# Kernel tuning notes

Hardware: AMD Instinct MI355X
Metric: run time of the kernel (lower is better)

## Reference

```python
import jax, jax.numpy as jnp
import numpy as np

EPS = 1e-6
NUM_CHANNELS = 8


def rotate_half(x):
    h = x.shape[-1] // 2
    return jnp.concatenate([-x[..., h:], x[..., :h]], axis=-1)


def l1_normalize(x):
    # torch F.normalize(p=1): x / max(||x||_1, eps) along last dim
    n = jnp.sum(jnp.abs(x), axis=-1, keepdims=True)
    return x / jnp.maximum(n, EPS)


def squared_softmax(x):      # potential_func_z = 'square'
    return l1_normalize(x * x)


def abs_normalization(x):    # potential_func_g = 'abs'
    return l1_normalize(jax.nn.relu(x))


def head_selection(qz, u, v, cos, sin):
    b, s, d = qz.shape
    C = NUM_CHANNELS
    r = u.shape[0] // C
    cos_e = cos[:, None]  # [b,1,s,r] (unsqueeze_dim=1)
    sin_e = sin[:, None]
    ap = lambda x: x * cos_e + rotate_half(x) * sin_e
    ap_o = lambda x: x * cos_e - rotate_half(x) * sin_e
    # [b,s,C*r] -> [b,C,s,r]
    qz_u = (qz @ u.T).reshape(b, s, C, r).transpose(0, 2, 1, 3)
    qz_v = (qz @ v.T).reshape(b, s, C, r).transpose(0, 2, 1, 3)
    qz_uo = ap_o(qz_u)
    qz_u = ap(qz_u)
    qz_v = ap(qz_v)
    msg_F = jnp.einsum('bcqr,bckr->bcqk', qz_u, qz_v)          # [b,C,s,s]
    # regularize_h = 1/dim_z -> softmax(F * dim_z)
    qh = jax.nn.softmax(msg_F.astype(jnp.float32) * d, axis=-1).astype(qz_u.dtype)
    qh_v1 = jnp.einsum('bcqk,bckr->bcqr', qh, qz_v)
    qh_v2 = jnp.einsum('bcqk,bcqr->bckr', qh, qz_uo)           # qh^T @ qz_uo
    qh_v1 = ap_o(qh_v1).transpose(0, 2, 1, 3).reshape(b, s, C * r)
    qh_v2 = ap(qh_v2).transpose(0, 2, 1, 3).reshape(b, s, C * r)
    return qh_v1 @ u + qh_v2 @ v                               # ternary_factor_scaling = 1


def topic_modeling(qz, w):
    qg = abs_normalization(qz @ w.T)     # binary_factor_scaling = regularize_g = 1
    return qg @ w


def period_message(qz, period_mat, period_attn):
    # info = P @ qz @ A, single term since _lambda = 0
    return jnp.einsum('qk,bkd->bqd', period_mat, qz) @ period_attn


def reference(unary, cos, sin, ternary_u, ternary_v, binary_factor,
              period_mat, period_attn, num_iters):
    # mean-field iterator: qz = act_z((unary + messages)/regularize_z), regularize_z = 1
    qz = squared_softmax(unary)
    for _ in range(num_iters):
        msg = (head_selection(qz, ternary_u, ternary_v, cos, sin)
               + topic_modeling(qz, binary_factor)
               + period_message(qz, period_mat, period_attn))
        qz = squared_softmax(unary + msg)
    return qz


def setup_inputs() -> dict:
    key = jax.random.key(0)
    ks = jax.random.split(key, 4)
    b, s, d, dff = 2, 2048, 256, 1024
    C = NUM_CHANNELS
    r = d // C  # head_dim = 32
    unary = jax.random.normal(ks[0], (b, s, d), dtype=jnp.float32)
    # RoPE tables (theta = 10000)
    inv_freq = 1.0 / (10000.0 ** (np.arange(0, r, 2, dtype=np.float32) / r))
    pos = np.arange(s, dtype=np.float32)
    freqs = pos[:, None] * inv_freq[None, :]
    emb = np.concatenate([freqs, freqs], axis=-1)               # [s, r]
    cos = jnp.broadcast_to(jnp.asarray(np.cos(emb))[None], (b, s, r)).astype(jnp.float32)
    sin = jnp.broadcast_to(jnp.asarray(np.sin(emb))[None], (b, s, r)).astype(jnp.float32)
    std = 0.2
    ternary_u = jax.random.normal(ks[1], (C * r, d), dtype=jnp.float32) * std
    ternary_v = jax.random.normal(ks[2], (C * r, d), dtype=jnp.float32) * std
    binary_factor = jax.random.normal(ks[3], (dff, d), dtype=jnp.float32) * std
    # PTPeriod buffers: band |i-j| == 24, and decaying matrix (k=1 -> identity)
    i = np.arange(s)
    period_mat = jnp.asarray((np.abs(i[:, None] - i[None, :]) == 24).astype(np.float32))
    j = np.arange(d)
    dist = np.abs(j[:, None] - j[None, :]).astype(np.float32)
    attn = np.exp(-0.5 * dist ** 2)
    attn[dist >= 1.0] = 0.0
    period_attn = jnp.asarray(attn, dtype=jnp.float32)
    return {"unary": unary, "cos": cos, "sin": sin,
            "ternary_u": ternary_u, "ternary_v": ternary_v,
            "binary_factor": binary_factor,
            "period_mat": period_mat, "period_attn": period_attn,
            "num_iters": 3}
```

## Files before the change

### kernel.cpp

```cpp
#include <hip/hip_runtime.h>
#include <math.h>

#define B 2
#define S 2048
#define D 256
#define DFF 1024
#define NC 8
#define R 32
#define NITER 3
#define EPSV 1e-6f
#define MROW (B * S)
#define NSPLIT 4

typedef unsigned short u16;
typedef unsigned int u32;
typedef __attribute__((ext_vector_type(8))) short short8_t;
typedef __attribute__((ext_vector_type(4))) float f32x4;

#define MFMA16(a, b, c) __builtin_amdgcn_mfma_f32_16x16x32_bf16(a, b, c, 0, 0, 0)

__device__ inline u16 bf16_rne(float x) {
  u32 u = __float_as_uint(x);
  u32 r = u + 0x7FFFu + ((u >> 16) & 1u);
  return (u16)(r >> 16);
}
__device__ inline void split2(float x, u16& h, u16& l) {
  h = bf16_rne(x);
  float hf = __uint_as_float(((u32)h) << 16);
  l = bf16_rne(x - hf);
}
__device__ inline short8_t ld8(const u16* p) { return *(const short8_t*)p; }

__device__ inline u32 pk2(float a, float b) {
  u32 r;
  asm("v_cvt_pk_bf16_f32 %0, %1, %2" : "=v"(r) : "v"(a), "v"(b));
  return r;
}
__device__ inline short8_t pack8(float c0, float c1, float c2, float c3,
                                 float c4, float c5, float c6, float c7) {
  union { u32 w[4]; short8_t v; } u_;
  u_.w[0] = pk2(c0, c1);
  u_.w[1] = pk2(c2, c3);
  u_.w[2] = pk2(c4, c5);
  u_.w[3] = pk2(c6, c7);
  return u_.v;
}

__device__ inline void gload_lds16(const u16* g, u16* l) {
  __builtin_amdgcn_global_load_lds(
      (const __attribute__((address_space(1))) unsigned int*)g,
      (__attribute__((address_space(3))) unsigned int*)l, 16, 0, 0);
}

__global__ __launch_bounds__(256) void k_sqsm(const float* __restrict__ unary,
                                              const float* __restrict__ msgs,
                                              const float* __restrict__ qzp,
                                              const int* __restrict__ pcols,
                                              const float* __restrict__ pvals,
                                              const int* __restrict__ pcnt,
                                              float* __restrict__ outf,
                                              u16* __restrict__ qzz) {
  int row = blockIdx.x;
  int t = threadIdx.x;
  int i = row * D + t;
  float x = unary[i];
  if (msgs) {
    const size_t NEl = (size_t)MROW * D;
#pragma unroll
    for (int p = 0; p < NSPLIT; p++) x += msgs[p * NEl + i];
    int b = row >> 11, q = row & 2047;
    int n = pcnt[q];
    for (int j = 0; j < n; j++)
      x = fmaf(pvals[q * 16 + j], qzp[(size_t)(b * S + pcols[q * 16 + j]) * D + t], x);
  }
  float v = x * x;
  float s = v;
#pragma unroll
  for (int off = 32; off; off >>= 1) s += __shfl_down(s, off, 64);
  __shared__ float red[4];
  if ((t & 63) == 0) red[t >> 6] = s;
  __syncthreads();
  float tot = fmaxf(red[0] + red[1] + red[2] + red[3], EPSV);
  float y = v / tot;
  if (outf) outf[i] = y;
  u16 h, l;
  split2(y, h, l);
  size_t rb = (size_t)row * 512;
  qzz[rb + t] = h;
  qzz[rb + 256 + t] = l;
}

__global__ __launch_bounds__(256) void k_gemm_z(
    const u16* __restrict__ Az, const u16* __restrict__ Bz,
    int K2, int Kpart, int N,
    float* __restrict__ outbase,
    float* __restrict__ quv, float* __restrict__ qg, float* __restrict__ qzp) {
  int Kh = K2 / 3;
  int Alda = Kh * 2;
  int m0 = blockIdx.x * 128, n0 = blockIdx.y * 128;
  int kbeg = blockIdx.z * Kpart, kend = kbeg + Kpart;
  int tid = threadIdx.x;
  int wid = tid >> 6, lane = tid & 63;
  int lr = lane & 15, lg = lane >> 4;
  int wm = (wid >> 1) * 64, wn = (wid & 1) * 64;

  __shared__ alignas(16) u16 As[8192];
  __shared__ alignas(16) u16 Bs[8192];

  f32x4 acc[4][4];
#pragma unroll
  for (int fr = 0; fr < 4; fr++)
#pragma unroll
    for (int fc = 0; fc < 4; fc++) acc[fr][fc] = (f32x4){0.f, 0.f, 0.f, 0.f};

  for (int kk = kbeg; kk < kend; kk += 64) {
    int zsrc = (kk >= Kh) ? kk - Kh : kk;
    __syncthreads();
#pragma unroll
    for (int it = 0; it < 4; it++) {
      int f = (it * 256 + tid) * 16;
      int row = f >> 7;
      int c16 = ((f >> 4) & 7) ^ (row & 7);
      u16* ldst = (u16*)As + it * 2048 + wid * 512;
      gload_lds16(Az + (size_t)(m0 + row) * Alda + zsrc + c16 * 8, ldst);
      u16* ldstB = (u16*)Bs + it * 2048 + wid * 512;
      gload_lds16(Bz + (size_t)(n0 + row) * K2 + kk + c16 * 8, ldstB);
    }
    __syncthreads();
#pragma unroll
    for (int ks = 0; ks < 2; ks++) {
      int cb = ks * 4 + lg;
      int sw = (cb ^ (lr & 7)) << 3;
      short8_t af[4], bf[4];
#pragma unroll
      for (int fr = 0; fr < 4; fr++)
        af[fr] = *(const short8_t*)(As + ((wm + fr * 16 + lr) << 6) + sw);
#pragma unroll
      for (int fc = 0; fc < 4; fc++)
        bf[fc] = *(const short8_t*)(Bs + ((wn + fc * 16 + lr) << 6) + sw);
      __builtin_amdgcn_s_setprio(1);
#pragma unroll
      for (int fr = 0; fr < 4; fr++)
#pragma unroll
        for (int fc = 0; fc < 4; fc++)
          acc[fr][fc] = MFMA16(af[fr], bf[fc], acc[fr][fc]);
      __builtin_amdgcn_s_setprio(0);
    }
  }

  if (qg) {
#pragma unroll
    for (int fr = 0; fr < 4; fr++)
#pragma unroll
      for (int fc = 0; fc < 4; fc++)
#pragma unroll
        for (int i = 0; i < 4; i++) {
          int m = m0 + wm + fr * 16 + lg * 4 + i;
          int nn = n0 + wn + fc * 16 + lr;
          float x = acc[fr][fc][i];
          if (nn < 512) quv[(size_t)m * 512 + nn] = x;
          else if (nn < 1536) qg[(size_t)m * DFF + nn - 512] = fmaxf(x, 0.f);
          else qzp[(size_t)m * 256 + nn - 1536] = x;
        }
  } else {
    float* out = outbase + (size_t)blockIdx.z * ((size_t)gridDim.x * 128) * N;
#pragma unroll
    for (int fr = 0; fr < 4; fr++)
#pragma unroll
      for (int fc = 0; fc < 4; fc++)
#pragma unroll
        for (int i = 0; i < 4; i++) {
          int m = m0 + wm + fr * 16 + lg * 4 + i;
          int nn = n0 + wn + fc * 16 + lr;
          out[(size_t)m * N + nn] = acc[fr][fc][i];
        }
  }
}

__global__ __launch_bounds__(256) void k_rope_pre(
    const float* __restrict__ quv, const float* __restrict__ cosb,
    const float* __restrict__ sinb,
    u16* __restrict__ Ah, u16* __restrict__ Al,
    u16* __restrict__ Bvh, u16* __restrict__ Bvl,
    u16* __restrict__ BvTph, u16* __restrict__ AoTph) {
  int row = blockIdx.x;
  int b = row >> 11, s_ = row & 2047;
  int t = threadIdx.x, c = t >> 5, rr = t & 31;
  float qu = quv[(size_t)row * 512 + t];
  float qv = quv[(size_t)row * 512 + 256 + t];
  float ou = __shfl_xor(qu, 16, 64);
  float ov = __shfl_xor(qv, 16, 64);
  float ru = (rr < 16) ? -ou : ou;
  float rv = (rr < 16) ? -ov : ov;
  float cs = cosb[(size_t)(b * S + s_) * R + rr];
  float sn = sinb[(size_t)(b * S + s_) * R + rr];
  float a = (qu * cs + ru * sn) * 256.f;
  float ao = qu * cs - ru * sn;
  float bv = qv * cs + rv * sn;
  size_t o = ((size_t)(b * NC + c) * S + s_) * R + rr;
  int off = s_ & 63;
  int kt = off >> 4;
  int pp = (kt >> 1) * 32 + ((off >> 2) & 3) * 8 + (kt & 1) * 4 + (off & 3);
  size_t otp = ((size_t)(b * NC + c) * R + rr) * S + (size_t)((s_ & ~63) + pp);
  u16 h, l;
  split2(a, h, l);  Ah[o] = h;  Al[o] = l;
  split2(bv, h, l); Bvh[o] = h; Bvl[o] = l; BvTph[otp] = h;
  split2(ao, h, l); AoTph[otp] = h;
}

__global__ __launch_bounds__(512) void k_attn1_mfma(
    const u16* __restrict__ Ah, const u16* __restrict__ Al,
    const u16* __restrict__ Bvh, const u16* __restrict__ Bvl,
    const u16* __restrict__ BvTph,
    float* __restrict__ O1, float* __restrict__ mbuf, float* __restrict__ lbuf) {
  int bidx = blockIdx.x;
  int xcd = bidx & 7, wv = bidx >> 3;
  int bc = xcd * 2 + (wv & 1);
  int tile = wv >> 1;
  int tid = threadIdx.x;
  int wid = tid >> 6, lane = tid & 63;
  int lr = lane & 15, lg = lane >> 4;
  int w4 = wid & 3, kh = wid >> 2;
  int qr = tile * 128 + w4 * 32;
  const size_t ofs = (size_t)bc * S * R;
  const size_t ofsT = (size_t)bc * R * S;

  __shared__ alignas(16) u16 BvhS[2][2][2048];
  __shared__ alignas(16) u16 BvlS[2][2][2048];
  __shared__ alignas(16) u16 PvS[2][2][2048];
  __shared__ float cm_o[4][32][34];
  __shared__ float cm_m[4][32], cm_l[4][32];

  short8_t a_hi[2], a_lo[2];
#pragma unroll
  for (int t = 0; t < 2; t++) {
    a_hi[t] = ld8(Ah + ofs + (size_t)(qr + t * 16 + lr) * R + lg * 8);
    a_lo[t] = ld8(Al + ofs + (size_t)(qr + t * 16 + lr) * R + lg * 8);
  }

  f32x4 o[2][2];
#pragma unroll
  for (int t = 0; t < 2; t++) { o[t][0] = (f32x4){0,0,0,0}; o[t][1] = (f32x4){0,0,0,0}; }
  float m_q[2] = {-1e30f, -1e30f}, l_p[2] = {0.f, 0.f};

  int khs = tid >> 8;
  int pch = tid & 255;
  int r4 = pch >> 2, c4 = pch & 3;
  int r8 = pch >> 3, c8 = pch & 7;
  int wql = (wid & 3) * 512;

#define A1_STAGE(STEP, DB)                                                     \
  {                                                                            \
    int kb_ = khs * 1024 + (STEP) * 64;                                        \
    gload_lds16(Bvh + ofs + (size_t)(kb_ + r4) * R + c4 * 8, &BvhS[DB][khs][wql]); \
    gload_lds16(Bvl + ofs + (size_t)(kb_ + r4) * R + c4 * 8, &BvlS[DB][khs][wql]); \
    gload_lds16(BvTph + ofsT + (size_t)r8 * S + kb_ + c8 * 8, &PvS[DB][khs][wql]); \
  }

  A1_STAGE(0, 0);
  for (int step = 0; step < 16; step++) {
    int db = step & 1;
    __syncthreads();
    if (step + 1 < 16) A1_STAGE(step + 1, db ^ 1);

    short8_t sbH[4], sbL[4], pvb[4];
#pragma unroll
    for (int kt = 0; kt < 4; kt++) {
      int ro = (kt * 16 + lr) * 32 + lg * 8;
      sbH[kt] = ld8(&BvhS[db][kh][ro]);
      sbL[kt] = ld8(&BvlS[db][kh][ro]);
    }
#pragma unroll
    for (int j = 0; j < 4; j++)
      pvb[j] = ld8(&PvS[db][kh][((j & 1) * 16 + lr) * 64 + (j >> 1) * 32 + lg * 8]);

    f32x4 c[2][4];
    __builtin_amdgcn_s_setprio(1);
#pragma unroll
    for (int t = 0; t < 2; t++)
#pragma unroll
      for (int kt = 0; kt < 4; kt++) {
        f32x4 cc = {0.f, 0.f, 0.f, 0.f};
        cc = MFMA16(sbH[kt], a_hi[t], cc);
        cc = MFMA16(sbH[kt], a_lo[t], cc);
        cc = MFMA16(sbL[kt], a_hi[t], cc);
        c[t][kt] = cc;
      }
    __builtin_amdgcn_s_setprio(0);
    float mx0 = -1e30f, mx1 = -1e30f;
#pragma unroll
    for (int kt = 0; kt < 4; kt++)
#pragma unroll
      for (int i = 0; i < 4; i++) {
        mx0 = fmaxf(mx0, c[0][kt][i]);
        mx1 = fmaxf(mx1, c[1][kt][i]);
      }
    bool ok_ = (mx0 <= m_q[0] + 8.f) && (mx1 <= m_q[1] + 8.f);
    if (!__all((int)ok_)) {
#pragma unroll
      for (int t = 0; t < 2; t++) {
        float mxt = (t == 0) ? mx0 : mx1;
        mxt = fmaxf(mxt, __shfl_xor(mxt, 16, 64));
        mxt = fmaxf(mxt, __shfl_xor(mxt, 32, 64));
        float mnew = fmaxf(m_q[t], mxt);
        float sc = __expf(m_q[t] - mnew);
        m_q[t] = mnew;
        l_p[t] *= sc;
#pragma unroll
        for (int i = 0; i < 4; i++) {
          float s4 = __shfl(sc, (lane & 48) | (lg * 4 + i), 64);
          o[t][0][i] *= s4;
          o[t][1][i] *= s4;
        }
      }
    }
#pragma unroll
    for (int t = 0; t < 2; t++) {
      float ps = 0.f;
#pragma unroll
      for (int kt = 0; kt < 4; kt++)
#pragma unroll
        for (int i = 0; i < 4; i++) {
          c[t][kt][i] = __expf(c[t][kt][i] - m_q[t]);
          ps += c[t][kt][i];
        }
      l_p[t] += ps;
    }
    __builtin_amdgcn_s_setprio(1);
#pragma unroll
    for (int t = 0; t < 2; t++) {
      short8_t f0h = pack8(c[t][0][0], c[t][0][1], c[t][0][2], c[t][0][3],
                           c[t][1][0], c[t][1][1], c[t][1][2], c[t][1][3]);
      short8_t f1h = pack8(c[t][2][0], c[t][2][1], c[t][2][2], c[t][2][3],
                           c[t][3][0], c[t][3][1], c[t][3][2], c[t][3][3]);
      o[t][0] = MFMA16(f0h, pvb[0], o[t][0]);
      o[t][1] = MFMA16(f0h, pvb[1], o[t][1]);
      o[t][0] = MFMA16(f1h, pvb[2], o[t][0]);
      o[t][1] = MFMA16(f1h, pvb[3], o[t][1]);
    }
    __builtin_amdgcn_s_setprio(0);
  }

  float m4[2][4], l4[2][4];
#pragma unroll
  for (int t = 0; t < 2; t++) {
    float lq = l_p[t];
    lq += __shfl_xor(lq, 16, 64);
    lq += __shfl_xor(lq, 32, 64);
#pragma unroll
    for (int i = 0; i < 4; i++) {
      int src = (lane & 48) | (lg * 4 + i);
      m4[t][i] = __shfl(m_q[t], src, 64);
      l4[t][i] = __shfl(lq, src, 64);
    }
  }
  __syncthreads();
  if (kh == 1) {
#pragma unroll
    for (int t = 0; t < 2; t++)
#pragma unroll
      for (int i = 0; i < 4; i++) {
        int r_ = t * 16 + lg * 4 + i;
        cm_o[w4][r_][lr] = o[t][0][i];
        cm_o[w4][r_][lr + 16] = o[t][1][i];
        if (lr == 0) { cm_m[w4][r_] = m4[t][i]; cm_l[w4][r_] = l4[t][i]; }
      }
  }
  __syncthreads();
  if (kh == 0) {
#pragma unroll
    for (int t = 0; t < 2; t++)
#pragma unroll
      for (int i = 0; i < 4; i++) {
        int r_ = t * 16 + lg * 4 + i;
        int q = qr + r_;
        float mb = cm_m[w4][r_], lb = cm_l[w4][r_];
        float mN = fmaxf(m4[t][i], mb);
        float ea = __expf(m4[t][i] - mN), eb = __expf(mb - mN);
        float inv = 1.f / (l4[t][i] * ea + lb * eb);
        O1[ofs + (size_t)q * R + lr] = (o[t][0][i] * ea + cm_o[w4][r_][lr] * eb) * inv;
        O1[ofs + (size_t)q * R + 16 + lr] = (o[t][1][i] * ea + cm_o[w4][r_][lr + 16] * eb) * inv;
        if (lr == 0) {
          mbuf[(size_t)bc * S + q] = mN;
          lbuf[(size_t)bc * S + q] = inv;
        }
      }
  }
}

__global__ __launch_bounds__(512) void k_attn2_mfma(
    const u16* __restrict__ Ah, const u16* __restrict__ Al,
    const u16* __restrict__ Bvh, const u16* __restrict__ Bvl,
    const u16* __restrict__ AoTph,
    const float* __restrict__ mbuf, const float* __restrict__ lbuf,
    float* __restrict__ O2) {
  int bidx = blockIdx.x;
  int xcd = bidx & 7, wv = bidx >> 3;
  int bc = xcd * 2 + (wv & 1);
  int tile = wv >> 1;
  int tid = threadIdx.x;
  int wid = tid >> 6, lane = tid & 63;
  int lr = lane & 15, lg = lane >> 4;
  int w4 = wid & 3, qh = wid >> 2;
  int kr = tile * 128 + w4 * 32;
  const size_t ofs = (size_t)bc * S * R;
  const size_t ofsT = (size_t)bc * R * S;

  __shared__ alignas(16) u16 AhS[2][2][2048];
  __shared__ alignas(16) u16 AlS[2][2][2048];
  __shared__ alignas(16) u16 PvS[2][2][2048];
  __shared__ float cm[4][32][34];

  short8_t bv_hi[2], bv_lo[2];
#pragma unroll
  for (int t = 0; t < 2; t++) {
    bv_hi[t] = ld8(Bvh + ofs + (size_t)(kr + t * 16 + lr) * R + lg * 8);
    bv_lo[t] = ld8(Bvl + ofs + (size_t)(kr + t * 16 + lr) * R + lg * 8);
  }

  f32x4 o[2][2];
#pragma unroll
  for (int t = 0; t < 2; t++) { o[t][0] = (f32x4){0,0,0,0}; o[t][1] = (f32x4){0,0,0,0}; }

  int qhs = tid >> 8;
  int pch = tid & 255;
  int r4 = pch >> 2, c4 = pch & 3;
  int r8 = pch >> 3, c8 = pch & 7;
  int wql = (wid & 3) * 512;

#define A2_STAGE(STEP, DB)                                                     \
  {                                                                            \
    int qb_ = qhs * 1024 + (STEP) * 64;                                        \
    gload_lds16(Ah + ofs + (size_t)(qb_ + r4) * R + c4 * 8, &AhS[DB][qhs][wql]);   \
    gload_lds16(Al + ofs + (size_t)(qb_ + r4) * R + c4 * 8, &AlS[DB][qhs][wql]);   \
    gload_lds16(AoTph + ofsT + (size_t)r8 * S + qb_ + c8 * 8, &PvS[DB][qhs][wql]); \
  }

  A2_STAGE(0, 0);
  for (int step = 0; step < 16; step++) {
    int db = step & 1;
    __syncthreads();
    if (step + 1 < 16) A2_STAGE(step + 1, db ^ 1);

    short8_t saH[4], saL[4], pvb[4];
#pragma unroll
    for (int qt = 0; qt < 4; qt++) {
      int ro = (qt * 16 + lr) * 32 + lg * 8;
      saH[qt] = ld8(&AhS[db][qh][ro]);
      saL[qt] = ld8(&AlS[db][qh][ro]);
    }
#pragma unroll
    for (int j = 0; j < 4; j++)
      pvb[j] = ld8(&PvS[db][qh][((j & 1) * 16 + lr) * 64 + (j >> 1) * 32 + lg * 8]);

    f32x4 c[2][4];
    __builtin_amdgcn_s_setprio(1);
#pragma unroll
    for (int t = 0; t < 2; t++)
#pragma unroll
      for (int qt = 0; qt < 4; qt++) {
        f32x4 cc = {0.f, 0.f, 0.f, 0.f};
        cc = MFMA16(saH[qt], bv_hi[t], cc);
        cc = MFMA16(saH[qt], bv_lo[t], cc);
        cc = MFMA16(saL[qt], bv_hi[t], cc);
        c[t][qt] = cc;
      }
    __builtin_amdgcn_s_setprio(0);
    size_t qa = (size_t)bc * S + qh * 1024 + step * 64;
    float4 mq0 = *(const float4*)(mbuf + qa + lg * 4);
    float4 mq1 = *(const float4*)(mbuf + qa + 16 + lg * 4);
    float4 mq2 = *(const float4*)(mbuf + qa + 32 + lg * 4);
    float4 mq3 = *(const float4*)(mbuf + qa + 48 + lg * 4);
    float4 il0 = *(const float4*)(lbuf + qa + lg * 4);
    float4 il1 = *(const float4*)(lbuf + qa + 16 + lg * 4);
    float4 il2 = *(const float4*)(lbuf + qa + 32 + lg * 4);
    float4 il3 = *(const float4*)(lbuf + qa + 48 + lg * 4);
#pragma unroll
    for (int t = 0; t < 2; t++) {
      c[t][0][0] = __expf(c[t][0][0] - mq0.x) * il0.x;
      c[t][0][1] = __expf(c[t][0][1] - mq0.y) * il0.y;
      c[t][0][2] = __expf(c[t][0][2] - mq0.z) * il0.z;
      c[t][0][3] = __expf(c[t][0][3] - mq0.w) * il0.w;
      c[t][1][0] = __expf(c[t][1][0] - mq1.x) * il1.x;
      c[t][1][1] = __expf(c[t][1][1] - mq1.y) * il1.y;
      c[t][1][2] = __expf(c[t][1][2] - mq1.z) * il1.z;
      c[t][1][3] = __expf(c[t][1][3] - mq1.w) * il1.w;
      c[t][2][0] = __expf(c[t][2][0] - mq2.x) * il2.x;
      c[t][2][1] = __expf(c[t][2][1] - mq2.y) * il2.y;
      c[t][2][2] = __expf(c[t][2][2] - mq2.z) * il2.z;
      c[t][2][3] = __expf(c[t][2][3] - mq2.w) * il2.w;
      c[t][3][0] = __expf(c[t][3][0] - mq3.x) * il3.x;
      c[t][3][1] = __expf(c[t][3][1] - mq3.y) * il3.y;
      c[t][3][2] = __expf(c[t][3][2] - mq3.z) * il3.z;
      c[t][3][3] = __expf(c[t][3][3] - mq3.w) * il3.w;
    }
    __builtin_amdgcn_s_setprio(1);
#pragma unroll
    for (int t = 0; t < 2; t++) {
      short8_t f0h = pack8(c[t][0][0], c[t][0][1], c[t][0][2], c[t][0][3],
                           c[t][1][0], c[t][1][1], c[t][1][2], c[t][1][3]);
      short8_t f1h = pack8(c[t][2][0], c[t][2][1], c[t][2][2], c[t][2][3],
                           c[t][3][0], c[t][3][1], c[t][3][2], c[t][3][3]);
      o[t][0] = MFMA16(f0h, pvb[0], o[t][0]);
      o[t][1] = MFMA16(f0h, pvb[1], o[t][1]);
      o[t][0] = MFMA16(f1h, pvb[2], o[t][0]);
      o[t][1] = MFMA16(f1h, pvb[3], o[t][1]);
    }
    __builtin_amdgcn_s_setprio(0);
  }

  __syncthreads();
  if (qh == 1) {
#pragma unroll
    for (int t = 0; t < 2; t++)
#pragma unroll
      for (int i = 0; i < 4; i++) {
        int r_ = t * 16 + lg * 4 + i;
        cm[w4][r_][lr] = o[t][0][i];
        cm[w4][r_][lr + 16] = o[t][1][i];
      }
  }
  __syncthreads();
  if (qh == 0) {
#pragma unroll
    for (int t = 0; t < 2; t++)
#pragma unroll
      for (int i = 0; i < 4; i++) {
        int r_ = t * 16 + lg * 4 + i;
        int k = kr + r_;
        O2[ofs + (size_t)k * R + lr] = o[t][0][i] + cm[w4][r_][lr];
        O2[ofs + (size_t)k * R + 16 + lr] = o[t][1][i] + cm[w4][r_][lr + 16];
      }
  }
}

__global__ __launch_bounds__(256) void k_post(const float* __restrict__ O1,
                                              const float* __restrict__ O2,
                                              const float* __restrict__ cosb,
                                              const float* __restrict__ sinb,
                                              const float* __restrict__ qg,
                                              u16* __restrict__ Abz) {
  int row = blockIdx.x;
  int b = row >> 11, s_ = row & 2047;
  int t = threadIdx.x, c = t >> 5, rr = t & 31;
  size_t base = ((size_t)(b * NC + c) * S + s_) * R;
  float x1 = O1[base + rr], x2 = O2[base + rr];
  float o1 = O1[base + (rr ^ 16)], o2 = O2[base + (rr ^ 16)];
  float r1 = (rr < 16) ? -o1 : o1;
  float r2 = (rr < 16) ? -o2 : o2;
  float cs = cosb[(size_t)(b * S + s_) * R + rr];
  float sn = sinb[(size_t)(b * S + s_) * R + rr];
  float v1 = x1 * cs - r1 * sn;
  float v2 = x2 * cs + r2 * sn;
  size_t rb = (size_t)row * 3072;
  u16 h, l;
  split2(v1, h, l);
  Abz[rb + t] = h;        Abz[rb + 1536 + t] = l;
  split2(v2, h, l);
  Abz[rb + 256 + t] = h;  Abz[rb + 1792 + t] = l;
  float vq[4];
  float s = 0.f;
#pragma unroll
  for (int j = 0; j < 4; j++) {
    vq[j] = qg[(size_t)row * DFF + t + 256 * j];
    s += vq[j];
  }
#pragma unroll
  for (int off = 32; off; off >>= 1) s += __shfl_down(s, off, 64);
  __shared__ float red[4];
  if ((t & 63) == 0) red[t >> 6] = s;
  __syncthreads();
  float inv = 1.f / fmaxf(red[0] + red[1] + red[2] + red[3], EPSV);
#pragma unroll
  for (int j = 0; j < 4; j++) {
    split2(vq[j] * inv, h, l);
    Abz[rb + 512 + t + 256 * j] = h;
    Abz[rb + 2048 + t + 256 * j] = l;
  }
}

__global__ __launch_bounds__(256) void k_prep_bt(const float* __restrict__ u,
                                                 const float* __restrict__ v,
                                                 const float* __restrict__ w,
                                                 const float* __restrict__ pa,
                                                 u16* __restrict__ btz) {
  int n = blockIdx.x;
  int k = threadIdx.x;
  float val = (n < 256)    ? u[(size_t)n * 256 + k]
            : (n < 512)    ? v[(size_t)(n - 256) * 256 + k]
            : (n < 1536)   ? w[(size_t)(n - 512) * 256 + k]
                           : pa[(size_t)k * 256 + (n - 1536)];
  u16 h, l;
  split2(val, h, l);
  size_t rb = (size_t)n * 768;
  btz[rb + k] = h;
  btz[rb + 256 + k] = l;
  btz[rb + 512 + k] = h;
}

__global__ __launch_bounds__(256) void k_prep_uvwT(const float* __restrict__ u,
                                                   const float* __restrict__ v,
                                                   const float* __restrict__ w,
                                                   u16* __restrict__ uvwTz) {
  int n = blockIdx.x;
  size_t rb = (size_t)n * 4608;
  for (int k = threadIdx.x; k < 1536; k += 256) {
    float val = (k < 256) ? u[(size_t)k * 256 + n]
              : (k < 512) ? v[(size_t)(k - 256) * 256 + n]
                          : w[(size_t)(k - 512) * 256 + n];
    u16 h, l;
    split2(val, h, l);
    uvwTz[rb + k] = h;
    uvwTz[rb + 1536 + k] = l;
    uvwTz[rb + 3072 + k] = h;
  }
}

__global__ __launch_bounds__(256) void k_pm_build(const float* __restrict__ pm,
                                                  int* __restrict__ cols,
                                                  float* __restrict__ vals,
                                                  int* __restrict__ cnt) {
  int q = blockIdx.x;
  int t = threadIdx.x;
  float v[8];
  int c = 0;
#pragma unroll
  for (int j = 0; j < 8; j++) {
    v[j] = pm[(size_t)q * S + t * 8 + j];
    c += (v[j] != 0.f) ? 1 : 0;
  }
  int lane = t & 63, w = t >> 6;
  int pc = c;
#pragma unroll
  for (int off = 1; off < 64; off <<= 1) {
    int o = __shfl_up(pc, off, 64);
    if (lane >= off) pc += o;
  }
  __shared__ int wsum[4];
  if (lane == 63) wsum[w] = pc;
  __syncthreads();
  int base = 0;
  for (int i = 0; i < w; i++) base += wsum[i];
  int idx = base + pc - c;
#pragma unroll
  for (int j = 0; j < 8; j++) {
    if (v[j] != 0.f) {
      if (idx < 16) {
        cols[q * 16 + idx] = t * 8 + j;
        vals[q * 16 + idx] = v[j];
      }
      idx++;
    }
  }
  if (t == 255) {
    int tot = base + pc;
    cnt[q] = tot > 16 ? 16 : tot;
  }
}

extern "C" void kernel_launch(void* const* d_in, const int* in_sizes, int n_in,
                              void* d_out, int out_size, void* d_ws, size_t ws_size,
                              hipStream_t stream) {
  const float* unary = (const float*)d_in[0];
  const float* cosb = (const float*)d_in[1];
  const float* sinb = (const float*)d_in[2];
  const float* u = (const float*)d_in[3];
  const float* v = (const float*)d_in[4];
  const float* w = (const float*)d_in[5];
  const float* pm = (const float*)d_in[6];
  const float* pa = (const float*)d_in[7];

  const size_t NE = (size_t)MROW * D;
  const size_t NB = (size_t)B * NC * S * R;

  float* fp = (float*)d_ws;
  float* msgs = fp;                fp += NSPLIT * NE;
  float* quv = fp;                 fp += 2 * NE;
  float* qg = fp;                  fp += 4 * NE;
  float* qzp = fp;                 fp += NE;
  float* mbuf = fp;                fp += B * NC * S;
  float* lbuf = fp;                fp += B * NC * S;
  float* pvals = fp;               fp += S * 16;
  int* pcols = (int*)fp;           fp += S * 16;
  int* pcnt = (int*)fp;            fp += S;
  float* O1 = quv;
  float* O2 = quv + NE;

  u16* bb = (u16*)fp;
  u16* qzz = bb;                   bb += (size_t)MROW * 512;
  u16* Abz = bb;                   bb += (size_t)MROW * 3072;
  u16* btz = bb;                   bb += (size_t)1792 * 768;
  u16* uvwTz = bb;                 bb += (size_t)256 * 4608;
  u16* Ah = bb;                    bb += NB;
  u16* Al = bb;                    bb += NB;
  u16* Bvh = bb;                   bb += NB;
  u16* Bvl = bb;                   bb += NB;
  u16* BvTph = bb;                 bb += NB;
  u16* AoTph = bb;                 bb += NB;

  k_pm_build<<<S, 256, 0, stream>>>(pm, pcols, pvals, pcnt);
  k_prep_bt<<<1792, 256, 0, stream>>>(u, v, w, pa, btz);
  k_prep_uvwT<<<256, 256, 0, stream>>>(u, v, w, uvwTz);

  k_sqsm<<<MROW, 256, 0, stream>>>(unary, nullptr, nullptr, nullptr, nullptr, nullptr,
                                   nullptr, qzz);

  for (int it = 0; it < NITER; ++it) {
    k_gemm_z<<<dim3(32, 14, 1), 256, 0, stream>>>(qzz, btz, 768, 768, 1792,
                                                  nullptr, quv, qg, qzp);
    k_rope_pre<<<MROW, 256, 0, stream>>>(quv, cosb, sinb, Ah, Al, Bvh, Bvl, BvTph, AoTph);
    k_attn1_mfma<<<256, 512, 0, stream>>>(Ah, Al, Bvh, Bvl, BvTph, O1, mbuf, lbuf);
    k_attn2_mfma<<<256, 512, 0, stream>>>(Ah, Al, Bvh, Bvl, AoTph, mbuf, lbuf, O2);
    k_post<<<MROW, 256, 0, stream>>>(O1, O2, cosb, sinb, qg, Abz);
    k_gemm_z<<<dim3(32, 2, NSPLIT), 256, 0, stream>>>(Abz, uvwTz, 4608, 4608 / NSPLIT, 256,
                                                      msgs, nullptr, nullptr, nullptr);
    k_sqsm<<<MROW, 256, 0, stream>>>(unary, msgs, qzp, pcols, pvals, pcnt,
                                     (it == NITER - 1) ? (float*)d_out : nullptr, qzz);
  }
}
```

Measured before the change: 454.2 us.

## Double waves per attention block, one 16-row tile per wave

Both attention kernels now launch 1024 threads (16 waves) per block instead of 512. Each wave handles a 16-row query or key tile instead of two 16-row tiles, and the cooperative LDS staging loads are repartitioned across the larger wave count. The goal is more waves per CU to hide latency on the serial softmax/exp and MFMA chains. In exchange, the same shared tiles are re-read from LDS by twice as many waves, and per-wave MFMA work per LDS read is halved.

```diff
diff --git a/kernel.cpp b/kernel.cpp
--- a/kernel.cpp
+++ b/kernel.cpp
@@ -208,7 +208,7 @@
   split2(ao, h, l); AoTph[otp] = h;
 }
 
-__global__ __launch_bounds__(512) void k_attn1_mfma(
+__global__ __launch_bounds__(1024) void k_attn1_mfma(
     const u16* __restrict__ Ah, const u16* __restrict__ Al,
     const u16* __restrict__ Bvh, const u16* __restrict__ Bvl,
     const u16* __restrict__ BvTph,
@@ -218,43 +218,41 @@
   int bc = xcd * 2 + (wv & 1);
   int tile = wv >> 1;
   int tid = threadIdx.x;
-  int wid = tid >> 6, lane = tid & 63;
+  int lane = tid & 63;
   int lr = lane & 15, lg = lane >> 4;
-  int w4 = wid & 3, kh = wid >> 2;
-  int qr = tile * 128 + w4 * 32;
+  int khs = tid >> 9;
+  int w8 = (tid >> 6) & 7;
+  int qr = tile * 128 + w8 * 16;
   const size_t ofs = (size_t)bc * S * R;
   const size_t ofsT = (size_t)bc * R * S;
 
   __shared__ alignas(16) u16 BvhS[2][2][2048];
   __shared__ alignas(16) u16 BvlS[2][2][2048];
   __shared__ alignas(16) u16 PvS[2][2][2048];
-  __shared__ float cm_o[4][32][34];
-  __shared__ float cm_m[4][32], cm_l[4][32];
-
-  short8_t a_hi[2], a_lo[2];
-#pragma unroll
-  for (int t = 0; t < 2; t++) {
-    a_hi[t] = ld8(Ah + ofs + (size_t)(qr + t * 16 + lr) * R + lg * 8);
-    a_lo[t] = ld8(Al + ofs + (size_t)(qr + t * 16 + lr) * R + lg * 8);
-  }
-
-  f32x4 o[2][2];
-#pragma unroll
-  for (int t = 0; t < 2; t++) { o[t][0] = (f32x4){0,0,0,0}; o[t][1] = (f32x4){0,0,0,0}; }
-  float m_q[2] = {-1e30f, -1e30f}, l_p[2] = {0.f, 0.f};
-
-  int khs = tid >> 8;
-  int pch = tid & 255;
-  int r4 = pch >> 2, c4 = pch & 3;
-  int r8 = pch >> 3, c8 = pch & 7;
-  int wql = (wid & 3) * 512;
-
-#define A1_STAGE(STEP, DB)                                                     \
-  {                                                                            \
-    int kb_ = khs * 1024 + (STEP) * 64;                                        \
-    gload_lds16(Bvh + ofs + (size_t)(kb_ + r4) * R + c4 * 8, &BvhS[DB][khs][wql]); \
-    gload_lds16(Bvl + ofs + (size_t)(kb_ + r4) * R + c4 * 8, &BvlS[DB][khs][wql]); \
-    gload_lds16(BvTph + ofsT + (size_t)r8 * S + kb_ + c8 * 8, &PvS[DB][khs][wql]); \
+  __shared__ float cm_o[8][16][34];
+  __shared__ float cm_m[8][16], cm_l[8][16];
+
+  short8_t a_hi = ld8(Ah + ofs + (size_t)(qr + lr) * R + lg * 8);
+  short8_t a_lo = ld8(Al + ofs + (size_t)(qr + lr) * R + lg * 8);
+
+  f32x4 o0 = {0, 0, 0, 0}, o1 = {0, 0, 0, 0};
+  float m_q = -1e30f, l_p = 0.f;
+
+  int ci = (w8 & 3) * 64 + lane;
+  int wql = (w8 & 3) * 512;
+
+#define A1_STAGE(STEP, DB)                                                         \
+  {                                                                                \
+    int kb_ = khs * 1024 + (STEP) * 64;                                            \
+    if (w8 < 4) {                                                                  \
+      gload_lds16(Bvh + ofs + (size_t)(kb_ + (ci >> 2)) * R + (ci & 3) * 8,        \
+                  &BvhS[DB][khs][wql]);                                            \
+      gload_lds16(BvTph + ofsT + (size_t)(ci >> 3) * S + kb_ + (ci & 7) * 8,       \
+                  &PvS[DB][khs][wql]);                                             \
+    } else {                                                                       \
+      gload_lds16(Bvl + ofs + (size_t)(kb_ + (ci >> 2)) * R + (ci & 3) * 8,        \
+                  &BvlS[DB][khs][wql]);                                            \
+    }                                                                              \
   }
 
   A1_STAGE(0, 0);
@@ -267,128 +265,105 @@
 #pragma unroll
     for (int kt = 0; kt < 4; kt++) {
       int ro = (kt * 16 + lr) * 32 + lg * 8;
-      sbH[kt] = ld8(&BvhS[db][kh][ro]);
-      sbL[kt] = ld8(&BvlS[db][kh][ro]);
+      sbH[kt] = ld8(&BvhS[db][khs][ro]);
+      sbL[kt] = ld8(&BvlS[db][khs][ro]);
     }
 #pragma unroll
     for (int j = 0; j < 4; j++)
-      pvb[j] = ld8(&PvS[db][kh][((j & 1) * 16 + lr) * 64 + (j >> 1) * 32 + lg * 8]);
-
-    f32x4 c[2][4];
+      pvb[j] = ld8(&PvS[db][khs][((j & 1) * 16 + lr) * 64 + (j >> 1) * 32 + lg * 8]);
+
+    f32x4 c[4];
     __builtin_amdgcn_s_setprio(1);
 #pragma unroll
-    for (int t = 0; t < 2; t++)
-#pragma unroll
-      for (int kt = 0; kt < 4; kt++) {
-        f32x4 cc = {0.f, 0.f, 0.f, 0.f};
-        cc = MFMA16(sbH[kt], a_hi[t], cc);
-        cc = MFMA16(sbH[kt], a_lo[t], cc);
-        cc = MFMA16(sbL[kt], a_hi[t], cc);
-        c[t][kt] = cc;
+    for (int kt = 0; kt < 4; kt++) {
+      f32x4 cc = {0.f, 0.f, 0.f, 0.f};
+      cc = MFMA16(sbH[kt], a_hi, cc);
+      cc = MFMA16(sbH[kt], a_lo, cc);
+      cc = MFMA16(sbL[kt], a_hi, cc);
+      c[kt] = cc;
+    }
+    __builtin_amdgcn_s_setprio(0);
+    float mx = -1e30f;
+#pragma unroll
+    for (int kt = 0; kt < 4; kt++)
+#pragma unroll
+      for (int i = 0; i < 4; i++) mx = fmaxf(mx, c[kt][i]);
+    if (!__all((int)(mx <= m_q + 8.f))) {
+      mx = fmaxf(mx, __shfl_xor(mx, 16, 64));
+      mx = fmaxf(mx, __shfl_xor(mx, 32, 64));
+      float mnew = fmaxf(m_q, mx);
+      float sc = __expf(m_q - mnew);
+      m_q = mnew;
+      l_p *= sc;
+#pragma unroll
+      for (int i = 0; i < 4; i++) {
+        float s4 = __shfl(sc, (lane & 48) | (lg * 4 + i), 64);
+        o0[i] *= s4;
+        o1[i] *= s4;
       }
+    }
+    float ps = 0.f;
+#pragma unroll
+    for (int kt = 0; kt < 4; kt++)
+#pragma unroll
+      for (int i = 0; i < 4; i++) {
+        c[kt][i] = __expf(c[kt][i] - m_q);
+        ps += c[kt][i];
+      }
+    l_p += ps;
+    __builtin_amdgcn_s_setprio(1);
+    short8_t f0h = pack8(c[0][0], c[0][1], c[0][2], c[0][3],
+                         c[1][0], c[1][1], c[1][2], c[1][3]);
+    short8_t f1h = pack8(c[2][0], c[2][1], c[2][2], c[2][3],
+                         c[3][0], c[3][1], c[3][2], c[3][3]);
+    o0 = MFMA16(f0h, pvb[0], o0);
+    o1 = MFMA16(f0h, pvb[1], o1);
+    o0 = MFMA16(f1h, pvb[2], o0);
+    o1 = MFMA16(f1h, pvb[3], o1);
     __builtin_amdgcn_s_setprio(0);
-    float mx0 = -1e30f, mx1 = -1e30f;
-#pragma unroll
-    for (int kt = 0; kt < 4; kt++)
-#pragma unroll
-      for (int i = 0; i < 4; i++) {
-        mx0 = fmaxf(mx0, c[0][kt][i]);
-        mx1 = fmaxf(mx1, c[1][kt][i]);
+  }
+
+  float lq = l_p;
+  lq += __shfl_xor(lq, 16, 64);
+  lq += __shfl_xor(lq, 32, 64);
+  float m4[4], l4[4];
+#pragma unroll
+  for (int i = 0; i < 4; i++) {
+    int src = (lane & 48) | (lg * 4 + i);
+    m4[i] = __shfl(m_q, src, 64);
+    l4[i] = __shfl(lq, src, 64);
+  }
+  __syncthreads();
+  if (khs == 1) {
+#pragma unroll
+    for (int i = 0; i < 4; i++) {
+      int r_ = lg * 4 + i;
+      cm_o[w8][r_][lr] = o0[i];
+      cm_o[w8][r_][lr + 16] = o1[i];
+      if (lr == 0) { cm_m[w8][r_] = m4[i]; cm_l[w8][r_] = l4[i]; }
+    }
+  }
+  __syncthreads();
+  if (khs == 0) {
+#pragma unroll
+    for (int i = 0; i < 4; i++) {
+      int r_ = lg * 4 + i;
+      int q = qr + r_;
+      float mb = cm_m[w8][r_], lb = cm_l[w8][r_];
+      float mN = fmaxf(m4[i], mb);
+      float ea = __expf(m4[i] - mN), eb = __expf(mb - mN);
+      float inv = 1.f / (l4[i] * ea + lb * eb);
+      O1[ofs + (size_t)q * R + lr] = (o0[i] * ea + cm_o[w8][r_][lr] * eb) * inv;
+      O1[ofs + (size_t)q * R + 16 + lr] = (o1[i] * ea + cm_o[w8][r_][lr + 16] * eb) * inv;
+      if (lr == 0) {
+        mbuf[(size_t)bc * S + q] = mN;
+        lbuf[(size_t)bc * S + q] = inv;
       }
-    bool ok_ = (mx0 <= m_q[0] + 8.f) && (mx1 <= m_q[1] + 8.f);
-    if (!__all((int)ok_)) {
-#pragma unroll
-      for (int t = 0; t < 2; t++) {
-        float mxt = (t == 0) ? mx0 : mx1;
-        mxt = fmaxf(mxt, __shfl_xor(mxt, 16, 64));
-        mxt = fmaxf(mxt, __shfl_xor(mxt, 32, 64));
-        float mnew = fmaxf(m_q[t], mxt);
-        float sc = __expf(m_q[t] - mnew);
-        m_q[t] = mnew;
-        l_p[t] *= sc;
-#pragma unroll
-        for (int i = 0; i < 4; i++) {
-          float s4 = __shfl(sc, (lane & 48) | (lg * 4 + i), 64);
-          o[t][0][i] *= s4;
-          o[t][1][i] *= s4;
-        }
-      }
-    }
-#pragma unroll
-    for (int t = 0; t < 2; t++) {
-      float ps = 0.f;
-#pragma unroll
-      for (int kt = 0; kt < 4; kt++)
-#pragma unroll
-        for (int i = 0; i < 4; i++) {
-          c[t][kt][i] = __expf(c[t][kt][i] - m_q[t]);
-          ps += c[t][kt][i];
-        }
-      l_p[t] += ps;
-    }
-    __builtin_amdgcn_s_setprio(1);
-#pragma unroll
-    for (int t = 0; t < 2; t++) {
-      short8_t f0h = pack8(c[t][0][0], c[t][0][1], c[t][0][2], c[t][0][3],
-                           c[t][1][0], c[t][1][1], c[t][1][2], c[t][1][3]);
-      short8_t f1h = pack8(c[t][2][0], c[t][2][1], c[t][2][2], c[t][2][3],
-                           c[t][3][0], c[t][3][1], c[t][3][2], c[t][3][3]);
-      o[t][0] = MFMA16(f0h, pvb[0], o[t][0]);
-      o[t][1] = MFMA16(f0h, pvb[1], o[t][1]);
-      o[t][0] = MFMA16(f1h, pvb[2], o[t][0]);
-      o[t][1] = MFMA16(f1h, pvb[3], o[t][1]);
-    }
-    __builtin_amdgcn_s_setprio(0);
-  }
-
-  float m4[2][4], l4[2][4];
-#pragma unroll
-  for (int t = 0; t < 2; t++) {
-    float lq = l_p[t];
-    lq += __shfl_xor(lq, 16, 64);
-    lq += __shfl_xor(lq, 32, 64);
-#pragma unroll
-    for (int i = 0; i < 4; i++) {
-      int src = (lane & 48) | (lg * 4 + i);
-      m4[t][i] = __shfl(m_q[t], src, 64);
-      l4[t][i] = __shfl(lq, src, 64);
-    }
-  }
-  __syncthreads();
-  if (kh == 1) {
-#pragma unroll
-    for (int t = 0; t < 2; t++)
-#pragma unroll
-      for (int i = 0; i < 4; i++) {
-        int r_ = t * 16 + lg * 4 + i;
-        cm_o[w4][r_][lr] = o[t][0][i];
-        cm_o[w4][r_][lr + 16] = o[t][1][i];
-        if (lr == 0) { cm_m[w4][r_] = m4[t][i]; cm_l[w4][r_] = l4[t][i]; }
-      }
-  }
-  __syncthreads();
-  if (kh == 0) {
-#pragma unroll
-    for (int t = 0; t < 2; t++)
-#pragma unroll
-      for (int i = 0; i < 4; i++) {
-        int r_ = t * 16 + lg * 4 + i;
-        int q = qr + r_;
-        float mb = cm_m[w4][r_], lb = cm_l[w4][r_];
-        float mN = fmaxf(m4[t][i], mb);
-        float ea = __expf(m4[t][i] - mN), eb = __expf(mb - mN);
-        float inv = 1.f / (l4[t][i] * ea + lb * eb);
-        O1[ofs + (size_t)q * R + lr] = (o[t][0][i] * ea + cm_o[w4][r_][lr] * eb) * inv;
-        O1[ofs + (size_t)q * R + 16 + lr] = (o[t][1][i] * ea + cm_o[w4][r_][lr + 16] * eb) * inv;
-        if (lr == 0) {
-          mbuf[(size_t)bc * S + q] = mN;
-          lbuf[(size_t)bc * S + q] = inv;
-        }
-      }
-  }
-}
-
-__global__ __launch_bounds__(512) void k_attn2_mfma(
+    }
+  }
+}
+
+__global__ __launch_bounds__(1024) void k_attn2_mfma(
     const u16* __restrict__ Ah, const u16* __restrict__ Al,
     const u16* __restrict__ Bvh, const u16* __restrict__ Bvl,
     const u16* __restrict__ AoTph,
@@ -399,41 +374,39 @@
   int bc = xcd * 2 + (wv & 1);
   int tile = wv >> 1;
   int tid = threadIdx.x;
-  int wid = tid >> 6, lane = tid & 63;
+  int lane = tid & 63;
   int lr = lane & 15, lg = lane >> 4;
-  int w4 = wid & 3, qh = wid >> 2;
-  int kr = tile * 128 + w4 * 32;
+  int qhs = tid >> 9;
+  int w8 = (tid >> 6) & 7;
+  int kr = tile * 128 + w8 * 16;
   const size_t ofs = (size_t)bc * S * R;
   const size_t ofsT = (size_t)bc * R * S;
 
   __shared__ alignas(16) u16 AhS[2][2][2048];
   __shared__ alignas(16) u16 AlS[2][2][2048];
   __shared__ alignas(16) u16 PvS[2][2][2048];
-  __shared__ float cm[4][32][34];
-
-  short8_t bv_hi[2], bv_lo[2];
-#pragma unroll
-  for (int t = 0; t < 2; t++) {
-    bv_hi[t] = ld8(Bvh + ofs + (size_t)(kr + t * 16 + lr) * R + lg * 8);
-    bv_lo[t] = ld8(Bvl + ofs + (size_t)(kr + t * 16 + lr) * R + lg * 8);
-  }
-
-  f32x4 o[2][2];
-#pragma unroll
-  for (int t = 0; t < 2; t++) { o[t][0] = (f32x4){0,0,0,0}; o[t][1] = (f32x4){0,0,0,0}; }
-
-  int qhs = tid >> 8;
-  int pch = tid & 255;
-  int r4 = pch >> 2, c4 = pch & 3;
-  int r8 = pch >> 3, c8 = pch & 7;
-  int wql = (wid & 3) * 512;
-
-#define A2_STAGE(STEP, DB)                                                     \
-  {                                                                            \
-    int qb_ = qhs * 1024 + (STEP) * 64;                                        \
-    gload_lds16(Ah + ofs + (size_t)(qb_ + r4) * R + c4 * 8, &AhS[DB][qhs][wql]);   \
-    gload_lds16(Al + ofs + (size_t)(qb_ + r4) * R + c4 * 8, &AlS[DB][qhs][wql]);   \
-    gload_lds16(AoTph + ofsT + (size_t)r8 * S + qb_ + c8 * 8, &PvS[DB][qhs][wql]); \
+  __shared__ float cm[8][16][34];
+
+  short8_t bv_hi = ld8(Bvh + ofs + (size_t)(kr + lr) * R + lg * 8);
+  short8_t bv_lo = ld8(Bvl + ofs + (size_t)(kr + lr) * R + lg * 8);
+
+  f32x4 o0 = {0, 0, 0, 0}, o1 = {0, 0, 0, 0};
+
+  int ci = (w8 & 3) * 64 + lane;
+  int wql = (w8 & 3) * 512;
+
+#define A2_STAGE(STEP, DB)                                                         \
+  {                                                                                \
+    int qb_ = qhs * 1024 + (STEP) * 64;                                            \
+    if (w8 < 4) {                                                                  \
+      gload_lds16(Ah + ofs + (size_t)(qb_ + (ci >> 2)) * R + (ci & 3) * 8,         \
+                  &AhS[DB][qhs][wql]);                                             \
+      gload_lds16(AoTph + ofsT + (size_t)(ci >> 3) * S + qb_ + (ci & 7) * 8,       \
+                  &PvS[DB][qhs][wql]);                                             \
+    } else {                                                                       \
+      gload_lds16(Al + ofs + (size_t)(qb_ + (ci >> 2)) * R + (ci & 3) * 8,         \
+                  &AlS[DB][qhs][wql]);                                             \
+    }                                                                              \
   }
 
   A2_STAGE(0, 0);
@@ -446,27 +419,25 @@
 #pragma unroll
     for (int qt = 0; qt < 4; qt++) {
       int ro = (qt * 16 + lr) * 32 + lg * 8;
-      saH[qt] = ld8(&AhS[db][qh][ro]);
-      saL[qt] = ld8(&AlS[db][qh][ro]);
+      saH[qt] = ld8(&AhS[db][qhs][ro]);
+      saL[qt] = ld8(&AlS[db][qhs][ro]);
     }
 #pragma unroll
     for (int j = 0; j < 4; j++)
-      pvb[j] = ld8(&PvS[db][qh][((j & 1) * 16 + lr) * 64 + (j >> 1) * 32 + lg * 8]);
-
-    f32x4 c[2][4];
+      pvb[j] = ld8(&PvS[db][qhs][((j & 1) * 16 + lr) * 64 + (j >> 1) * 32 + lg * 8]);
+
+    f32x4 c[4];
     __builtin_amdgcn_s_setprio(1);
 #pragma unroll
-    for (int t = 0; t < 2; t++)
-#pragma unroll
-      for (int qt = 0; qt < 4; qt++) {
-        f32x4 cc = {0.f, 0.f, 0.f, 0.f};
-        cc = MFMA16(saH[qt], bv_hi[t], cc);
-        cc = MFMA16(saH[qt], bv_lo[t], cc);
-        cc = MFMA16(saL[qt], bv_hi[t], cc);
-        c[t][qt] = cc;
-      }
+    for (int qt = 0; qt < 4; qt++) {
+      f32x4 cc = {0.f, 0.f, 0.f, 0.f};
+      cc = MFMA16(saH[qt], bv_hi, cc);
+      cc = MFMA16(saH[qt], bv_lo, cc);
+      cc = MFMA16(saL[qt], bv_hi, cc);
+      c[qt] = cc;
+    }
     __builtin_amdgcn_s_setprio(0);
-    size_t qa = (size_t)bc * S + qh * 1024 + step * 64;
+    size_t qa = (size_t)bc * S + qhs * 1024 + step * 64;
     float4 mq0 = *(const float4*)(mbuf + qa + lg * 4);
     float4 mq1 = *(const float4*)(mbuf + qa + 16 + lg * 4);
     float4 mq2 = *(const float4*)(mbuf + qa + 32 + lg * 4);
@@ -475,62 +446,52 @@
     float4 il1 = *(const float4*)(lbuf + qa + 16 + lg * 4);
     float4 il2 = *(const float4*)(lbuf + qa + 32 + lg * 4);
     float4 il3 = *(const float4*)(lbuf + qa + 48 + lg * 4);
-#pragma unroll
-    for (int t = 0; t < 2; t++) {
-      c[t][0][0] = __expf(c[t][0][0] - mq0.x) * il0.x;
-      c[t][0][1] = __expf(c[t][0][1] - mq0.y) * il0.y;
-      c[t][0][2] = __expf(c[t][0][2] - mq0.z) * il0.z;
-      c[t][0][3] = __expf(c[t][0][3] - mq0.w) * il0.w;
-      c[t][1][0] = __expf(c[t][1][0] - mq1.x) * il1.x;
-      c[t][1][1] = __expf(c[t][1][1] - mq1.y) * il1.y;
-      c[t][1][2] = __expf(c[t][1][2] - mq1.z) * il1.z;
-      c[t][1][3] = __expf(c[t][1][3] - mq1.w) * il1.w;
-      c[t][2][0] = __expf(c[t][2][0] - mq2.x) * il2.x;
-      c[t][2][1] = __expf(c[t][2][1] - mq2.y) * il2.y;
-      c[t][2][2] = __expf(c[t][2][2] - mq2.z) * il2.z;
-      c[t][2][3] = __expf(c[t][2][3] - mq2.w) * il2.w;
-      c[t][3][0] = __expf(c[t][3][0] - mq3.x) * il3.x;
-      c[t][3][1] = __expf(c[t][3][1] - mq3.y) * il3.y;
-      c[t][3][2] = __expf(c[t][3][2] - mq3.z) * il3.z;
-      c[t][3][3] = __expf(c[t][3][3] - mq3.w) * il3.w;
-    }
+    c[0][0] = __expf(c[0][0] - mq0.x) * il0.x;
+    c[0][1] = __expf(c[0][1] - mq0.y) * il0.y;
+    c[0][2] = __expf(c[0][2] - mq0.z) * il0.z;
+    c[0][3] = __expf(c[0][3] - mq0.w) * il0.w;
+    c[1][0] = __expf(c[1][0] - mq1.x) * il1.x;
+    c[1][1] = __expf(c[1][1] - mq1.y) * il1.y;
+    c[1][2] = __expf(c[1][2] - mq1.z) * il1.z;
+    c[1][3] = __expf(c[1][3] - mq1.w) * il1.w;
+    c[2][0] = __expf(c[2][0] - mq2.x) * il2.x;
+    c[2][1] = __expf(c[2][1] - mq2.y) * il2.y;
+    c[2][2] = __expf(c[2][2] - mq2.z) * il2.z;
+    c[2][3] = __expf(c[2][3] - mq2.w) * il2.w;
+    c[3][0] = __expf(c[3][0] - mq3.x) * il3.x;
+    c[3][1] = __expf(c[3][1] - mq3.y) * il3.y;
+    c[3][2] = __expf(c[3][2] - mq3.z) * il3.z;
+    c[3][3] = __expf(c[3][3] - mq3.w) * il3.w;
     __builtin_amdgcn_s_setprio(1);
-#pragma unroll
-    for (int t = 0; t < 2; t++) {
-      short8_t f0h = pack8(c[t][0][0], c[t][0][1], c[t][0][2], c[t][0][3],
-                           c[t][1][0], c[t][1][1], c[t][1][2], c[t][1][3]);
-      short8_t f1h = pack8(c[t][2][0], c[t][2][1], c[t][2][2], c[t][2][3],
-                           c[t][3][0], c[t][3][1], c[t][3][2], c[t][3][3]);
-      o[t][0] = MFMA16(f0h, pvb[0], o[t][0]);
-      o[t][1] = MFMA16(f0h, pvb[1], o[t][1]);
-      o[t][0] = MFMA16(f1h, pvb[2], o[t][0]);
-      o[t][1] = MFMA16(f1h, pvb[3], o[t][1]);
-    }
+    short8_t f0h = pack8(c[0][0], c[0][1], c[0][2], c[0][3],
+                         c[1][0], c[1][1], c[1][2], c[1][3]);
+    short8_t f1h = pack8(c[2][0], c[2][1], c[2][2], c[2][3],
+                         c[3][0], c[3][1], c[3][2], c[3][3]);
+    o0 = MFMA16(f0h, pvb[0], o0);
+    o1 = MFMA16(f0h, pvb[1], o1);
+    o0 = MFMA16(f1h, pvb[2], o0);
+    o1 = MFMA16(f1h, pvb[3], o1);
     __builtin_amdgcn_s_setprio(0);
   }
 
   __syncthreads();
-  if (qh == 1) {
-#pragma unroll
-    for (int t = 0; t < 2; t++)
-#pragma unroll
-      for (int i = 0; i < 4; i++) {
-        int r_ = t * 16 + lg * 4 + i;
-        cm[w4][r_][lr] = o[t][0][i];
-        cm[w4][r_][lr + 16] = o[t][1][i];
-      }
+  if (qhs == 1) {
+#pragma unroll
+    for (int i = 0; i < 4; i++) {
+      int r_ = lg * 4 + i;
+      cm[w8][r_][lr] = o0[i];
+      cm[w8][r_][lr + 16] = o1[i];
+    }
   }
   __syncthreads();
-  if (qh == 0) {
-#pragma unroll
-    for (int t = 0; t < 2; t++)
-#pragma unroll
-      for (int i = 0; i < 4; i++) {
-        int r_ = t * 16 + lg * 4 + i;
-        int k = kr + r_;
-        O2[ofs + (size_t)k * R + lr] = o[t][0][i] + cm[w4][r_][lr];
-        O2[ofs + (size_t)k * R + 16 + lr] = o[t][1][i] + cm[w4][r_][lr + 16];
-      }
+  if (qhs == 0) {
+#pragma unroll
+    for (int i = 0; i < 4; i++) {
+      int r_ = lg * 4 + i;
+      int k = kr + r_;
+      O2[ofs + (size_t)k * R + lr] = o0[i] + cm[w8][r_][lr];
+      O2[ofs + (size_t)k * R + 16 + lr] = o1[i] + cm[w8][r_][lr + 16];
+    }
   }
 }
 
@@ -709,8 +670,8 @@
     k_gemm_z<<<dim3(32, 14, 1), 256, 0, stream>>>(qzz, btz, 768, 768, 1792,
                                                   nullptr, quv, qg, qzp);
     k_rope_pre<<<MROW, 256, 0, stream>>>(quv, cosb, sinb, Ah, Al, Bvh, Bvl, BvTph, AoTph);
-    k_attn1_mfma<<<256, 512, 0, stream>>>(Ah, Al, Bvh, Bvl, BvTph, O1, mbuf, lbuf);
-    k_attn2_mfma<<<256, 512, 0, stream>>>(Ah, Al, Bvh, Bvl, AoTph, mbuf, lbuf, O2);
+    k_attn1_mfma<<<256, 1024, 0, stream>>>(Ah, Al, Bvh, Bvl, BvTph, O1, mbuf, lbuf);
+    k_attn2_mfma<<<256, 1024, 0, stream>>>(Ah, Al, Bvh, Bvl, AoTph, mbuf, lbuf, O2);
     k_post<<<MROW, 256, 0, stream>>>(O1, O2, cosb, sinb, qg, Abz);
     k_gemm_z<<<dim3(32, 2, NSPLIT), 256, 0, stream>>>(Abz, uvwTz, 4608, 4608 / NSPLIT, 256,
                                                       msgs, nullptr, nullptr, nullptr);
```

After: 451.2 us. About the same (-0.7%).
